# Kernel optimization log

Hardware: AMD Instinct MI355X
Metric: run time of the kernel (lower is better)

The kernel has to match this reference:

```python
import jax, jax.numpy as jnp
import numpy as np

B, N, D, H, DH, FF, CI, K, MPE = 8, 1024, 512, 8, 64, 2048, 1024, 31, 512
PAD = (K // 2, K // 2 - (K + 1) % 2)  # (15, 15)


def _ln(x, g, b):
    m = x.mean(-1, keepdims=True)
    v = ((x - m) ** 2).mean(-1, keepdims=True)
    return (x - m) * jax.lax.rsqrt(v + 1e-5) * g + b


def _swish(x):
    return x * jax.nn.sigmoid(x)


def setup_inputs() -> dict:
    key = jax.random.key(0)
    ks = iter(jax.random.split(key, 40))
    def w(shape, s=0.02):
        return (jax.random.normal(next(ks), shape) * s).astype(jnp.float32)
    ones = lambda n: jnp.ones((n,), jnp.float32)
    zeros = lambda n: jnp.zeros((n,), jnp.float32)
    return dict(
        x=jax.random.normal(next(ks), (B, N, D), dtype=jnp.float32),
        f1_g=ones(D), f1_b=zeros(D), f1_w1=w((D, FF)), f1_b1=zeros(FF), f1_w2=w((FF, D)), f1_b2=zeros(D),
        a_g=ones(D), a_b=zeros(D), wq=w((D, H * DH)), wkv=w((D, 2 * H * DH)), wo=w((H * DH, D)), wo_b=zeros(D),
        rel=w((2 * MPE + 1, DH)),
        c_g=ones(D), c_b=zeros(D), cw1=w((D, 2 * CI)), cb1=zeros(2 * CI), dw=w((CI, K)), db=zeros(CI),
        bn_g=ones(CI), bn_b=zeros(CI), bn_m=zeros(CI), bn_v=ones(CI), cw2=w((CI, D)), cb2=zeros(D),
        f2_g=ones(D), f2_b=zeros(D), f2_w1=w((D, FF)), f2_b1=zeros(FF), f2_w2=w((FF, D)), f2_b2=zeros(D),
        p_g=ones(D), p_b=zeros(D),
    )


def reference(x, f1_g, f1_b, f1_w1, f1_b1, f1_w2, f1_b2,
              a_g, a_b, wq, wkv, wo, wo_b, rel,
              c_g, c_b, cw1, cb1, dw, db, bn_g, bn_b, bn_m, bn_v, cw2, cb2,
              f2_g, f2_b, f2_w1, f2_b1, f2_w2, f2_b2, p_g, p_b):
    # FF1 (half-step)
    h = _ln(x, f1_g, f1_b)
    x = x + 0.5 * (_swish(h @ f1_w1 + f1_b1) @ f1_w2 + f1_b2)
    # Attention with relative positional bias
    h = _ln(x, a_g, a_b)
    q = (h @ wq).reshape(B, N, H, DH).transpose(0, 2, 1, 3)          # bhnd
    k, v = jnp.split(h @ wkv, 2, axis=-1)
    k = k.reshape(B, N, H, DH).transpose(0, 2, 1, 3)
    v = v.reshape(B, N, H, DH).transpose(0, 2, 1, 3)
    scale = DH ** -0.5
    dots = jnp.einsum('bhid,bhjd->bhij', q, k) * scale
    seq = jnp.arange(N)
    dist = jnp.clip(seq[:, None] - seq[None, :], -MPE, MPE) + MPE    # [N,N]
    rp = rel[dist]                                                   # [N,N,DH]
    dots = dots + jnp.einsum('bhnd,nrd->bhnr', q, rp) * scale
    attn = jax.nn.softmax(dots, axis=-1)
    o = jnp.einsum('bhij,bhjd->bhid', attn, v).transpose(0, 2, 1, 3).reshape(B, N, H * DH)
    x = x + o @ wo + wo_b
    # Conv module: LN -> pw conv -> GLU -> depthwise conv -> BN(eval) -> swish -> pw conv
    h = _ln(x, c_g, c_b)
    h = h @ cw1 + cb1                                                # [B,N,2CI]
    out, gate = jnp.split(h, 2, axis=-1)
    h = (out * jax.nn.sigmoid(gate)).transpose(0, 2, 1)              # [B,CI,N]
    h = jnp.pad(h, ((0, 0), (0, 0), PAD))
    h = jax.lax.conv_general_dilated(h, dw[:, None, :], (1,), 'VALID',
                                     feature_group_count=CI,
                                     dimension_numbers=('NCH', 'OIH', 'NCH')) + db[None, :, None]
    h = (h - bn_m[None, :, None]) * jax.lax.rsqrt(bn_v[None, :, None] + 1e-5) * bn_g[None, :, None] + bn_b[None, :, None]
    h = _swish(h).transpose(0, 2, 1)                                 # [B,N,CI]
    x = x + h @ cw2 + cb2
    # FF2 (half-step) + post norm
    h = _ln(x, f2_g, f2_b)
    x = x + 0.5 * (_swish(h @ f2_w1 + f2_b1) @ f2_w2 + f2_b2)
    return _ln(x, p_g, p_b)
```

## Files before the change

kernel.cpp:

```cpp
#include <hip/hip_runtime.h>
#include <hip/hip_bf16.h>
#include <cstdint>


using bf16_t = __hip_bfloat16;
typedef __bf16 bf16x8 __attribute__((ext_vector_type(8)));
typedef float floatx4 __attribute__((ext_vector_type(4)));

struct alignas(16) hbf8 { bf16_t h[8]; };
struct alignas(8)  hbf4 { bf16_t h[4]; };

__device__ __forceinline__ float  b2f(bf16_t h) { return __bfloat162float(h); }
__device__ __forceinline__ bf16_t f2b(float f)  { return __float2bfloat16(f); }
__device__ __forceinline__ float  sig_(float x) { return 1.f / (1.f + __expf(-x)); }

__device__ __forceinline__ void async16(const void* g, void* l) {
  __builtin_amdgcn_global_load_lds(
      (const __attribute__((address_space(1))) unsigned int*)(uintptr_t)g,
      (__attribute__((address_space(3))) unsigned int*)(uintptr_t)l, 16, 0, 0);
}

struct GemmArgs {
  const bf16_t* A; const bf16_t* Bt; const float* bias; const float* srcf;
  bf16_t* C; float* resid;
  int K, lda, ldb, ldc;
  long sAb, sAh, sBb, sBh, sCb, sCh;
  float alpha, beta;
};

template <int BM, int BN, int WR, int WC, int EPI>
__global__ __launch_bounds__(256) void gemm_bt(GemmArgs g) {
  constexpr int FM = BM / (WR * 16);
  constexpr int FN = BN / (WC * 16);
  constexpr int IA = (BM * 4) / 256;
  constexpr int IB = (BN * 4) / 256;
  __shared__ __align__(16) bf16_t As[BM * 32];
  __shared__ __align__(16) bf16_t Bs[BN * 32];
  const int tid = threadIdx.x;
  const int lane = tid & 63, w = tid >> 6;
  int bx = blockIdx.x, by = blockIdx.y;
  {
    const int gx = gridDim.x;
    const int nwg = gx * gridDim.y;
    if ((nwg & 7) == 0 && gridDim.z == 1) {
      int lin = by * gx + bx;
      int lid = (lin & 7) * (nwg >> 3) + (lin >> 3);
      bx = lid % gx; by = lid / gx;
    }
  }
  const int bm0 = by * BM, bn0 = bx * BN;
  const int zb = blockIdx.z >> 3, zh = blockIdx.z & 7;
  const bf16_t* Ab = g.A + (long)zb * g.sAb + (long)zh * g.sAh;
  const bf16_t* Bb = g.Bt + (long)zb * g.sBb + (long)zh * g.sBh;
  const int wm0 = (w / WC) * (FM * 16);
  const int wn0 = (w % WC) * (FN * 16);
  const int lrow = lane & 15, lq = lane >> 4;

  floatx4 acc[FM][FN] = {};

  for (int k0 = 0; k0 < g.K; k0 += 32) {
#pragma unroll
    for (int i = 0; i < IA; ++i) {
      int c = i * 256 + tid;
      int m = c >> 2, kk = (c & 3) * 8;
      async16(Ab + (long)(bm0 + m) * g.lda + (k0 + kk), (char*)As + c * 16);
    }
#pragma unroll
    for (int i = 0; i < IB; ++i) {
      int c = i * 256 + tid;
      int n = bn0 + (c >> 2), kk = (c & 3) * 8;
      async16(Bb + (long)n * g.ldb + (k0 + kk), (char*)Bs + c * 16);
    }
    __syncthreads();
    bf16x8 af[FM], bfr[FN];
#pragma unroll
    for (int fm = 0; fm < FM; ++fm)
      af[fm] = *(const bf16x8*)(As + (wm0 + fm * 16 + lrow) * 32 + lq * 8);
#pragma unroll
    for (int fn = 0; fn < FN; ++fn)
      bfr[fn] = *(const bf16x8*)(Bs + (wn0 + fn * 16 + lrow) * 32 + lq * 8);
#pragma unroll
    for (int fm = 0; fm < FM; ++fm)
#pragma unroll
      for (int fn = 0; fn < FN; ++fn)
        acc[fm][fn] = __builtin_amdgcn_mfma_f32_16x16x32_bf16(af[fm], bfr[fn], acc[fm][fn], 0, 0, 0);
    __syncthreads();
  }

  const int bi = bm0 + wm0 + lq * 4;
  const int bj = bn0 + wn0 + lrow;
  if constexpr (EPI == 2) {
    float* R = g.resid;
    const float* S = g.srcf;
#pragma unroll
    for (int fm = 0; fm < FM; ++fm)
#pragma unroll
      for (int fn = 0; fn < FN; ++fn) {
        int j = bj + fn * 16;
        float bv = g.bias ? g.bias[j] : 0.f;
#pragma unroll
        for (int r = 0; r < 4; ++r) {
          long i = bi + fm * 16 + r;
          float base = S ? S[i * g.ldc + j] : R[i * g.ldc + j];
          R[i * g.ldc + j] = base + g.beta * (acc[fm][fn][r] + bv);
        }
      }
  } else if constexpr (EPI == 4) {
    bf16_t* C = g.C;
#pragma unroll
    for (int fm = 0; fm < FM; ++fm)
#pragma unroll
      for (int fn = 0; fn < FN; ++fn) {
        int j = bj + fn * 16;
        float bv = g.bias[(j >> 1) + (j & 1) * 1024];
#pragma unroll
        for (int r = 0; r < 4; ++r) {
          int i = bi + fm * 16 + r;
          float v = acc[fm][fn][r] + bv;
          float gp = __shfl_xor(v, 1);
          if ((j & 1) == 0)
            C[(long)i * g.ldc + (j >> 1)] = f2b(v * sig_(gp));
        }
      }
  } else {
    bf16_t* C = g.C + (long)zb * g.sCb + (long)zh * g.sCh;
#pragma unroll
    for (int fm = 0; fm < FM; ++fm)
#pragma unroll
      for (int fn = 0; fn < FN; ++fn) {
        int j = bj + fn * 16;
        float bv = g.bias ? g.bias[j] : 0.f;
#pragma unroll
        for (int r = 0; r < 4; ++r) {
          int i = bi + fm * 16 + r;
          float v = acc[fm][fn][r];
          if constexpr (EPI == 0) v = g.alpha * v + bv;
          if constexpr (EPI == 1) { v += bv; v = v * sig_(v); }
          C[(long)i * g.ldc + j] = f2b(v);
        }
      }
  }
}

__global__ __launch_bounds__(512, 4) void attn_kernel(
    const bf16_t* __restrict__ QKV, const bf16_t* __restrict__ VT,
    const bf16_t* __restrict__ RELP, bf16_t* __restrict__ O) {
  constexpr int LDT = 1028;
  __shared__ __align__(16) bf16_t Tls[32 * LDT];
  __shared__ float scr[576];

  const int tid = threadIdx.x;
  const int w = tid >> 6, lane = tid & 63;
  const int lrow = lane & 15, lq = lane >> 4;
  const int lin = blockIdx.y * gridDim.x + blockIdx.x;
  const int lid = (lin & 7) * 256 + (lin >> 3);
  const int z = lid >> 5;
  const int i0 = (lid & 31) * 32;
  const int b = z >> 3, zh = z & 7;
  const int j0w = w * 128;

  const bf16_t* Qb  = QKV + ((long)(b * 1024 + i0)) * 1536 + zh * 64;
  const bf16_t* Kb  = QKV + ((long)b * 1024) * 1536 + 512 + zh * 64;
  const bf16_t* VTb = VT + ((long)(b * 8 + zh)) * 65536;

  bf16x8 af[2][2];
#pragma unroll
  for (int fm = 0; fm < 2; ++fm)
#pragma unroll
    for (int ks = 0; ks < 2; ++ks)
      af[fm][ks] = *(const bf16x8*)(Qb + (long)(fm * 16 + lrow) * 1536 + ks * 32 + lq * 8);

  {
    const int u0w = w * 144;
    bf16x8 rf[18];
#pragma unroll
    for (int fnT = 0; fnT < 9; ++fnT) {
      const int u0 = u0w + fnT * 16;
      if (u0 < LDT) {
        rf[2 * fnT]     = *(const bf16x8*)(RELP + (long)(u0 + lrow) * 64 + lq * 8);
        rf[2 * fnT + 1] = *(const bf16x8*)(RELP + (long)(u0 + lrow) * 64 + 32 + lq * 8);
      }
    }
#pragma unroll
    for (int fnT = 0; fnT < 9; ++fnT) {
      const int u0 = u0w + fnT * 16;
      if (u0 < LDT) {
        floatx4 tacc[2] = {};
        tacc[0] = __builtin_amdgcn_mfma_f32_16x16x32_bf16(af[0][0], rf[2 * fnT],     tacc[0], 0, 0, 0);
        tacc[0] = __builtin_amdgcn_mfma_f32_16x16x32_bf16(af[0][1], rf[2 * fnT + 1], tacc[0], 0, 0, 0);
        tacc[1] = __builtin_amdgcn_mfma_f32_16x16x32_bf16(af[1][0], rf[2 * fnT],     tacc[1], 0, 0, 0);
        tacc[1] = __builtin_amdgcn_mfma_f32_16x16x32_bf16(af[1][1], rf[2 * fnT + 1], tacc[1], 0, 0, 0);
        const int uu = u0 + lrow;
#pragma unroll
        for (int fm = 0; fm < 2; ++fm)
#pragma unroll
          for (int r = 0; r < 4; ++r)
            if (uu < LDT)
              Tls[(fm * 16 + lq * 4 + r) * LDT + uu] = f2b(tacc[fm][r]);
      }
    }
  }

  bf16x8 kfA[8], kfB[8];
#pragma unroll
  for (int x = 0; x < 8; ++x)
    kfA[x] = *(const bf16x8*)(Kb + (long)(j0w + (x >> 1) * 16 + lrow) * 1536 + (x & 1) * 32 + lq * 8);
#pragma unroll
  for (int x = 0; x < 8; ++x)
    kfB[x] = *(const bf16x8*)(Kb + (long)(j0w + (4 + (x >> 1)) * 16 + lrow) * 1536 + (x & 1) * 32 + lq * 8);
  __syncthreads();

  floatx4 sacc[2][8] = {};
#pragma unroll
  for (int fn = 0; fn < 4; ++fn) {
    sacc[0][fn] = __builtin_amdgcn_mfma_f32_16x16x32_bf16(af[0][0], kfA[2 * fn],     sacc[0][fn], 0, 0, 0);
    sacc[0][fn] = __builtin_amdgcn_mfma_f32_16x16x32_bf16(af[0][1], kfA[2 * fn + 1], sacc[0][fn], 0, 0, 0);
    sacc[1][fn] = __builtin_amdgcn_mfma_f32_16x16x32_bf16(af[1][0], kfA[2 * fn],     sacc[1][fn], 0, 0, 0);
    sacc[1][fn] = __builtin_amdgcn_mfma_f32_16x16x32_bf16(af[1][1], kfA[2 * fn + 1], sacc[1][fn], 0, 0, 0);
  }
#pragma unroll
  for (int fn = 4; fn < 8; ++fn) {
    sacc[0][fn] = __builtin_amdgcn_mfma_f32_16x16x32_bf16(af[0][0], kfB[2 * (fn - 4)],     sacc[0][fn], 0, 0, 0);
    sacc[0][fn] = __builtin_amdgcn_mfma_f32_16x16x32_bf16(af[0][1], kfB[2 * (fn - 4) + 1], sacc[0][fn], 0, 0, 0);
    sacc[1][fn] = __builtin_amdgcn_mfma_f32_16x16x32_bf16(af[1][0], kfB[2 * (fn - 4)],     sacc[1][fn], 0, 0, 0);
    sacc[1][fn] = __builtin_amdgcn_mfma_f32_16x16x32_bf16(af[1][1], kfB[2 * (fn - 4) + 1], sacc[1][fn], 0, 0, 0);
  }

#pragma unroll
  for (int fm = 0; fm < 2; ++fm)
#pragma unroll
    for (int r = 0; r < 4; ++r) {
      const int il = fm * 16 + lq * 4 + r;
      const bf16_t* trow = Tls + il * LDT + 512;
      const int tb = i0 + il - j0w - lrow;
#pragma unroll
      for (int fn = 0; fn < 8; ++fn) {
        int t = tb - fn * 16;
        t = t < -512 ? -512 : (t > 512 ? 512 : t);
        sacc[fm][fn][r] += b2f(trow[t]);
      }
    }

  float rmax[2][4];
#pragma unroll
  for (int fm = 0; fm < 2; ++fm)
#pragma unroll
    for (int r = 0; r < 4; ++r) {
      float m = sacc[fm][0][r];
#pragma unroll
      for (int fn = 1; fn < 8; ++fn) m = fmaxf(m, sacc[fm][fn][r]);
      rmax[fm][r] = m;
    }
#pragma unroll
  for (int off = 1; off < 16; off <<= 1)
#pragma unroll
    for (int fm = 0; fm < 2; ++fm)
#pragma unroll
      for (int r = 0; r < 4; ++r)
        rmax[fm][r] = fmaxf(rmax[fm][r], __shfl_xor(rmax[fm][r], off));
  if (lrow == 0)
#pragma unroll
    for (int fm = 0; fm < 2; ++fm)
#pragma unroll
      for (int r = 0; r < 4; ++r)
        scr[(fm * 16 + lq * 4 + r) * 9 + w] = rmax[fm][r];
  __syncthreads();

  float rsum[2][4];
#pragma unroll
  for (int fm = 0; fm < 2; ++fm)
#pragma unroll
    for (int r = 0; r < 4; ++r) {
      const float* rr = scr + (fm * 16 + lq * 4 + r) * 9;
      float m = rr[0];
#pragma unroll
      for (int ww = 1; ww < 8; ++ww) m = fmaxf(m, rr[ww]);
      float s = 0.f;
#pragma unroll
      for (int fn = 0; fn < 8; ++fn) {
        float e = __expf(sacc[fm][fn][r] - m);
        sacc[fm][fn][r] = e;
        s += e;
      }
      rsum[fm][r] = s;
    }
#pragma unroll
  for (int off = 1; off < 16; off <<= 1)
#pragma unroll
    for (int fm = 0; fm < 2; ++fm)
#pragma unroll
      for (int r = 0; r < 4; ++r)
        rsum[fm][r] += __shfl_xor(rsum[fm][r], off);
  if (lrow == 0)
#pragma unroll
    for (int fm = 0; fm < 2; ++fm)
#pragma unroll
      for (int r = 0; r < 4; ++r)
        scr[288 + (fm * 16 + lq * 4 + r) * 9 + w] = rsum[fm][r];
  __syncthreads();

  float inv[2][4];
#pragma unroll
  for (int fm = 0; fm < 2; ++fm)
#pragma unroll
    for (int r = 0; r < 4; ++r) {
      const float* rr = scr + 288 + (fm * 16 + lq * 4 + r) * 9;
      float s = rr[0];
#pragma unroll
      for (int ww = 1; ww < 8; ++ww) s += rr[ww];
      inv[fm][r] = 1.f / s;
    }

  bf16x8 vfA[8];
#pragma unroll
  for (int x = 0; x < 8; ++x)
    vfA[x] = *(const bf16x8*)(VTb + (long)((x & 3) * 16 + lrow) * 1024 + j0w + (x >> 2) * 32 + lq * 8);

#pragma unroll
  for (int fm = 0; fm < 2; ++fm)
#pragma unroll
    for (int fn = 0; fn < 8; ++fn)
#pragma unroll
      for (int r = 0; r < 4; ++r) {
        const int i = fm * 16 + lq * 4 + r;
        const int j = j0w + fn * 16 + lrow;
        const unsigned boff = (unsigned)(i * 2048 + j * 2) ^ ((unsigned)(i & 7) << 4);
        *(bf16_t*)((char*)Tls + boff) = f2b(sacc[fm][fn][r] * inv[fm][r]);
      }

  bf16x8 vfB[8];
#pragma unroll
  for (int x = 0; x < 8; ++x)
    vfB[x] = *(const bf16x8*)(VTb + (long)((x & 3) * 16 + lrow) * 1024 + j0w + 64 + (x >> 2) * 32 + lq * 8);

  floatx4 oacc[2][4] = {};
#pragma unroll
  for (int ks = 0; ks < 4; ++ks) {
    const int j = j0w + ks * 32;
    bf16x8 ap[2];
#pragma unroll
    for (int fm = 0; fm < 2; ++fm) {
      const int i = fm * 16 + lrow;
      const unsigned boff = (unsigned)(i * 2048 + (j + lq * 8) * 2) ^ ((unsigned)(i & 7) << 4);
      ap[fm] = *(const bf16x8*)((char*)Tls + boff);
    }
#pragma unroll
    for (int fd = 0; fd < 4; ++fd) {
      bf16x8 bv = (ks < 2) ? vfA[(ks << 2) | fd] : vfB[((ks - 2) << 2) | fd];
      oacc[0][fd] = __builtin_amdgcn_mfma_f32_16x16x32_bf16(ap[0], bv, oacc[0][fd], 0, 0, 0);
      oacc[1][fd] = __builtin_amdgcn_mfma_f32_16x16x32_bf16(ap[1], bv, oacc[1][fd], 0, 0, 0);
    }
  }
  __syncthreads();

  {
    float* part = (float*)Tls + w * 2048;
#pragma unroll
    for (int fm = 0; fm < 2; ++fm)
#pragma unroll
      for (int fd = 0; fd < 4; ++fd)
#pragma unroll
        for (int r = 0; r < 4; ++r)
          part[(fm * 16 + lq * 4 + r) * 64 + fd * 16 + lrow] = oacc[fm][fd][r];
  }
  __syncthreads();

  {
    const int i = tid >> 4;
    const int d0 = (tid & 15) * 4;
    floatx4 s = {};
#pragma unroll
    for (int ww = 0; ww < 8; ++ww)
      s += *(const floatx4*)((const float*)Tls + ww * 2048 + i * 64 + d0);
    hbf4 o4;
#pragma unroll
    for (int m = 0; m < 4; ++m) o4.h[m] = f2b(s[m]);
    *(hbf4*)(O + (long)(b * 1024 + i0 + i) * 512 + zh * 64 + d0) = o4;
  }
}

__global__ __launch_bounds__(256) void diag_kernel(float* __restrict__ out, long n, float v) {
  long i = (long)blockIdx.x * 256 + threadIdx.x;
  if (i < n) out[i] = v;
}

__global__ __launch_bounds__(256) void relpad_kernel(const float* __restrict__ rel, bf16_t* __restrict__ RELP) {
  int i = blockIdx.x * 256 + threadIdx.x;
  if (i < 73728) {
    int r = i >> 6, c = i & 63;
    RELP[i] = (r < 1025) ? f2b(rel[r * 64 + c]) : f2b(0.f);
  }
}

template <bool F32OUT>
__global__ __launch_bounds__(256) void ln_kernel(const float* __restrict__ X, const float* __restrict__ gam,
                                                 const float* __restrict__ bet, void* __restrict__ outv) {
  int row = blockIdx.x, tid = threadIdx.x;
  const float* x = X + (long)row * 512;
  float a = x[tid], b = x[tid + 256];
  float s = a + b, q = a * a + b * b;
  for (int off = 32; off; off >>= 1) { s += __shfl_down(s, off); q += __shfl_down(q, off); }
  __shared__ float red[8];
  int w = tid >> 6;
  if ((tid & 63) == 0) { red[w] = s; red[w + 4] = q; }
  __syncthreads();
  float ts = red[0] + red[1] + red[2] + red[3];
  float tq = red[4] + red[5] + red[6] + red[7];
  float mean = ts * (1.f / 512.f);
  float var = tq * (1.f / 512.f) - mean * mean;
  float rs = rsqrtf(var + 1e-5f);
  float o0 = (a - mean) * rs * gam[tid]       + bet[tid];
  float o1 = (b - mean) * rs * gam[tid + 256] + bet[tid + 256];
  if constexpr (F32OUT) {
    float* out = (float*)outv;
    out[(long)row * 512 + tid]       = o0;
    out[(long)row * 512 + tid + 256] = o1;
  } else {
    bf16_t* out = (bf16_t*)outv;
    out[(long)row * 512 + tid]       = f2b(o0);
    out[(long)row * 512 + tid + 256] = f2b(o1);
  }
}

__global__ __launch_bounds__(256) void transpose_kernel(const float* __restrict__ in, bf16_t* __restrict__ out,
                                                        int R, int C, float scale, int perm) {
  __shared__ float t[32][33];
  int c0 = blockIdx.x * 32, r0 = blockIdx.y * 32;
  int tx = threadIdx.x & 31, ty = threadIdx.x >> 5;
#pragma unroll
  for (int i = 0; i < 4; ++i)
    t[ty + i * 8][tx] = in[(long)(r0 + ty + i * 8) * C + c0 + tx];
  __syncthreads();
#pragma unroll
  for (int i = 0; i < 4; ++i) {
    int c = c0 + ty + i * 8;
    int row = perm ? ((c < 1024) ? 2 * c : 2 * (c - 1024) + 1) : c;
    out[(long)row * R + r0 + tx] = f2b(t[tx][ty + i * 8] * scale);
  }
}

__global__ __launch_bounds__(256) void vt_kernel(const bf16_t* __restrict__ QKV, bf16_t* __restrict__ VT) {
  int jb = blockIdx.x, z = blockIdx.y;
  int b = z >> 3, h = z & 7;
  const bf16_t* src = QKV + (long)b * 1024 * 1536 + 1024 + h * 64;
  bf16_t* dst = VT + (long)z * 65536;
  __shared__ bf16_t t[64][65];
  int tid = threadIdx.x;
#pragma unroll
  for (int i = 0; i < 16; ++i) {
    int l = i * 256 + tid;
    int j = l >> 6, d = l & 63;
    t[d][j] = src[(long)(jb * 64 + j) * 1536 + d];
  }
  __syncthreads();
#pragma unroll
  for (int i = 0; i < 16; ++i) {
    int l = i * 256 + tid;
    int d = l >> 6, j = l & 63;
    dst[(long)d * 1024 + jb * 64 + j] = t[d][j];
  }
}

__global__ __launch_bounds__(256) void dwconv_kernel(const bf16_t* __restrict__ G, const float* __restrict__ dw,
    const float* __restrict__ db, const float* __restrict__ bng, const float* __restrict__ bnb,
    const float* __restrict__ bnm, const float* __restrict__ bnv, bf16_t* __restrict__ out) {
  int n0 = blockIdx.x * 32, c0 = blockIdx.y * 64, b = blockIdx.z;
  __shared__ bf16_t t[62][64];
  __shared__ float dws[31][64];
  int tid = threadIdx.x;
  const bf16_t* src = G + (long)b * 1024 * 1024 + c0;
#pragma unroll
  for (int i = 0; i < 16; ++i) {
    int l = i * 256 + tid;
    if (l < 3968) {
      int rr = l >> 6, c = l & 63;
      int n = n0 - 15 + rr;
      t[rr][c] = (n >= 0 && n < 1024) ? src[(long)n * 1024 + c] : f2b(0.f);
    }
  }
#pragma unroll
  for (int i = 0; i < 8; ++i) {
    int l = i * 256 + tid;
    if (l < 1984) {
      int k = l >> 6, c = l & 63;
      dws[k][c] = dw[(long)(c0 + c) * 31 + k];
    }
  }
  __syncthreads();
  int c = tid & 63, nl = tid >> 6;
  float rs = rsqrtf(bnv[c0 + c] + 1e-5f);
  float sc = rs * bng[c0 + c];
  float ab = (db[c0 + c] - bnm[c0 + c]) * sc + bnb[c0 + c];
#pragma unroll
  for (int j = 0; j < 8; ++j) {
    int rr = nl * 8 + j;
    float s = 0.f;
#pragma unroll
    for (int k = 0; k < 31; ++k) s += b2f(t[rr + k][c]) * dws[k][c];
    float y = s * sc + ab;
    out[((long)b * 1024 + n0 + rr) * 1024 + c0 + c] = f2b(y * sig_(y));
  }
}

extern "C" void kernel_launch(void* const* d_in, const int* in_sizes, int n_in,
                              void* d_out, int out_size, void* d_ws, size_t ws_size,
                              hipStream_t stream) {
  auto fail = [&](float code) {
    diag_kernel<<<(out_size + 255) / 256, 256, 0, stream>>>((float*)d_out, out_size, code);
  };
  if (n_in != 34)             { fail(70.f);  return; }
  if (in_sizes[0] != 4194304) { fail(80.f);  return; }

  const float* x     = (const float*)d_in[0];
  const float* f1_g  = (const float*)d_in[1];
  const float* f1_b  = (const float*)d_in[2];
  const float* f1_w1 = (const float*)d_in[3];
  const float* f1_b1 = (const float*)d_in[4];
  const float* f1_w2 = (const float*)d_in[5];
  const float* f1_b2 = (const float*)d_in[6];
  const float* a_g   = (const float*)d_in[7];
  const float* a_b   = (const float*)d_in[8];
  const float* wq    = (const float*)d_in[9];
  const float* wkv   = (const float*)d_in[10];
  const float* wo    = (const float*)d_in[11];
  const float* wo_b  = (const float*)d_in[12];
  const float* rel   = (const float*)d_in[13];
  const float* c_g   = (const float*)d_in[14];
  const float* c_b   = (const float*)d_in[15];
  const float* cw1   = (const float*)d_in[16];
  const float* cb1   = (const float*)d_in[17];
  const float* dwp   = (const float*)d_in[18];
  const float* dbp   = (const float*)d_in[19];
  const float* bn_g  = (const float*)d_in[20];
  const float* bn_b  = (const float*)d_in[21];
  const float* bn_m  = (const float*)d_in[22];
  const float* bn_v  = (const float*)d_in[23];
  const float* cw2   = (const float*)d_in[24];
  const float* cb2   = (const float*)d_in[25];
  const float* f2_g  = (const float*)d_in[26];
  const float* f2_b  = (const float*)d_in[27];
  const float* f2_w1 = (const float*)d_in[28];
  const float* f2_b1 = (const float*)d_in[29];
  const float* f2_w2 = (const float*)d_in[30];
  const float* f2_b2 = (const float*)d_in[31];
  const float* p_g   = (const float*)d_in[32];
  const float* p_b   = (const float*)d_in[33];

  char* ws = (char*)d_ws;
  const size_t OFF_X  = 0;
  const size_t OFF_WT = 16777216;
  const size_t OFF_D  = 30408704;
  const size_t OFF_E  = 63963136;
  const size_t relp_off = OFF_E + 33554432;
  if (ws_size < relp_off + 147456ULL) { fail(200.f); return; }

  float*  X   = (float*)(ws + OFF_X);
  bf16_t* WT  = (bf16_t*)(ws + OFF_WT);
  bf16_t* QKV = (bf16_t*)(ws + OFF_D);
  bf16_t* VT  = (bf16_t*)(ws + OFF_D + 25165824);
  bf16_t* GLU = (bf16_t*)(ws + OFF_D);
  bf16_t* DWO = (bf16_t*)(ws + OFF_D + 16777216);
  bf16_t* MID = (bf16_t*)(ws + OFF_E);
  bf16_t* RELP= (bf16_t*)(ws + relp_off);
  bf16_t* H   = (bf16_t*)d_out;
  bf16_t* O   = (bf16_t*)d_out;

  bf16_t* f1_w1t = WT;            bf16_t* f1_w2t = WT + 1048576;
  bf16_t* wqkvt  = WT + 2097152;
  bf16_t* wot    = WT + 2883584;  bf16_t* cw1t   = WT + 3145728;
  bf16_t* cw2t   = WT + 4194304;  bf16_t* f2_w1t = WT + 4718592;
  bf16_t* f2_w2t = WT + 5767168;

  auto GA = [](const bf16_t* A, const bf16_t* Bt, const float* bias, bf16_t* C,
               float* resid, const float* srcf, int K, int lda, int ldb, int ldc,
               float alpha, float beta) {
    GemmArgs g{}; g.A = A; g.Bt = Bt; g.bias = bias; g.srcf = srcf; g.C = C; g.resid = resid;
    g.K = K; g.lda = lda; g.ldb = ldb; g.ldc = ldc;
    g.sAb = g.sAh = g.sBb = g.sBh = g.sCb = g.sCh = 0; g.alpha = alpha; g.beta = beta;
    return g;
  };
  auto T = [&](const float* in, bf16_t* out, int R, int C, float scale = 1.f, int perm = 0) {
    transpose_kernel<<<dim3(C / 32, R / 32), 256, 0, stream>>>(in, out, R, C, scale, perm);
  };

  relpad_kernel<<<288, 256, 0, stream>>>(rel, RELP);
  T(f1_w1, f1_w1t, 512, 2048);        T(f1_w2, f1_w2t, 2048, 512);
  T(wq, wqkvt, 512, 512, 0.125f);     T(wkv, wqkvt + 262144, 512, 1024);
  T(wo, wot, 512, 512);               T(cw1, cw1t, 512, 2048, 1.f, 1);
  T(cw2, cw2t, 1024, 512);            T(f2_w1, f2_w1t, 512, 2048);
  T(f2_w2, f2_w2t, 2048, 512);

  ln_kernel<false><<<8192, 256, 0, stream>>>(x, f1_g, f1_b, H);
  { GemmArgs g = GA(H, f1_w1t, f1_b1, MID, nullptr, nullptr, 512, 512, 512, 2048, 1.f, 0.f);
    gemm_bt<128, 128, 2, 2, 1><<<dim3(16, 64, 1), 256, 0, stream>>>(g); }
  { GemmArgs g = GA(MID, f1_w2t, f1_b2, nullptr, X, x, 2048, 2048, 2048, 512, 1.f, 0.5f);
    gemm_bt<64, 128, 1, 4, 2><<<dim3(4, 128, 1), 256, 0, stream>>>(g); }

  ln_kernel<false><<<8192, 256, 0, stream>>>(X, a_g, a_b, H);
  { GemmArgs g = GA(H, wqkvt, nullptr, QKV, nullptr, nullptr, 512, 512, 512, 1536, 1.f, 0.f);
    gemm_bt<128, 128, 2, 2, 0><<<dim3(12, 64, 1), 256, 0, stream>>>(g); }
  vt_kernel<<<dim3(16, 64), 256, 0, stream>>>(QKV, VT);

  attn_kernel<<<dim3(32, 64), 512, 0, stream>>>(QKV, VT, RELP, O);

  { GemmArgs g = GA(O, wot, wo_b, nullptr, X, nullptr, 512, 512, 512, 512, 1.f, 1.f);
    gemm_bt<64, 128, 1, 4, 2><<<dim3(4, 128, 1), 256, 0, stream>>>(g); }

  ln_kernel<false><<<8192, 256, 0, stream>>>(X, c_g, c_b, H);
  { GemmArgs g = GA(H, cw1t, cb1, GLU, nullptr, nullptr, 512, 512, 512, 1024, 1.f, 0.f);
    gemm_bt<128, 128, 2, 2, 4><<<dim3(16, 64, 1), 256, 0, stream>>>(g); }
  dwconv_kernel<<<dim3(32, 16, 8), 256, 0, stream>>>(GLU, dwp, dbp, bn_g, bn_b, bn_m, bn_v, DWO);
  { GemmArgs g = GA(DWO, cw2t, cb2, nullptr, X, nullptr, 1024, 1024, 1024, 512, 1.f, 1.f);
    gemm_bt<64, 128, 1, 4, 2><<<dim3(4, 128, 1), 256, 0, stream>>>(g); }

  ln_kernel<false><<<8192, 256, 0, stream>>>(X, f2_g, f2_b, H);
  { GemmArgs g = GA(H, f2_w1t, f2_b1, MID, nullptr, nullptr, 512, 512, 512, 2048, 1.f, 0.f);
    gemm_bt<128, 128, 2, 2, 1><<<dim3(16, 64, 1), 256, 0, stream>>>(g); }
  { GemmArgs g = GA(MID, f2_w2t, f2_b2, nullptr, X, nullptr, 2048, 2048, 2048, 512, 1.f, 0.5f);
    gemm_bt<64, 128, 1, 4, 2><<<dim3(4, 128, 1), 256, 0, stream>>>(g); }
  ln_kernel<true><<<8192, 256, 0, stream>>>(X, p_g, p_b, (float*)d_out);
}
```

Baseline: 643.5 us.

## Defer softmax normalization to cross-wave merge and batch weight prep into one launch

Attention softmax now uses each wave's local row max and sum instead of a block-wide max and sum, which removes two __syncthreads barriers. The per-wave partial outputs are then rescaled by exp(local max minus global max) and normalized during the final cross-wave reduction, as in flash-style merging. Separately, the nine weight transposes and the relpad conversion are merged into a single prep_kernel launch driven by a job table, which cuts launch overhead. The cost is some extra exp and multiply work in the reduction and a per-block linear search over the job table.

```diff
diff --git a/kernel.cpp b/kernel.cpp
--- a/kernel.cpp
+++ b/kernel.cpp
@@ -264,21 +264,16 @@
 #pragma unroll
       for (int r = 0; r < 4; ++r)
         scr[(fm * 16 + lq * 4 + r) * 9 + w] = rmax[fm][r];
-  __syncthreads();
 
   float rsum[2][4];
 #pragma unroll
   for (int fm = 0; fm < 2; ++fm)
 #pragma unroll
     for (int r = 0; r < 4; ++r) {
-      const float* rr = scr + (fm * 16 + lq * 4 + r) * 9;
-      float m = rr[0];
-#pragma unroll
-      for (int ww = 1; ww < 8; ++ww) m = fmaxf(m, rr[ww]);
       float s = 0.f;
 #pragma unroll
       for (int fn = 0; fn < 8; ++fn) {
-        float e = __expf(sacc[fm][fn][r] - m);
+        float e = __expf(sacc[fm][fn][r] - rmax[fm][r]);
         sacc[fm][fn][r] = e;
         s += e;
       }
@@ -297,24 +292,13 @@
 #pragma unroll
       for (int r = 0; r < 4; ++r)
         scr[288 + (fm * 16 + lq * 4 + r) * 9 + w] = rsum[fm][r];
-  __syncthreads();
-
-  float inv[2][4];
-#pragma unroll
-  for (int fm = 0; fm < 2; ++fm)
-#pragma unroll
-    for (int r = 0; r < 4; ++r) {
-      const float* rr = scr + 288 + (fm * 16 + lq * 4 + r) * 9;
-      float s = rr[0];
-#pragma unroll
-      for (int ww = 1; ww < 8; ++ww) s += rr[ww];
-      inv[fm][r] = 1.f / s;
-    }
 
   bf16x8 vfA[8];
 #pragma unroll
   for (int x = 0; x < 8; ++x)
     vfA[x] = *(const bf16x8*)(VTb + (long)((x & 3) * 16 + lrow) * 1024 + j0w + (x >> 2) * 32 + lq * 8);
+
+  __syncthreads();
 
 #pragma unroll
   for (int fm = 0; fm < 2; ++fm)
@@ -325,7 +309,7 @@
         const int i = fm * 16 + lq * 4 + r;
         const int j = j0w + fn * 16 + lrow;
         const unsigned boff = (unsigned)(i * 2048 + j * 2) ^ ((unsigned)(i & 7) << 4);
-        *(bf16_t*)((char*)Tls + boff) = f2b(sacc[fm][fn][r] * inv[fm][r]);
+        *(bf16_t*)((char*)Tls + boff) = f2b(sacc[fm][fn][r]);
       }
 
   bf16x8 vfB[8];
@@ -368,13 +352,28 @@
   {
     const int i = tid >> 4;
     const int d0 = (tid & 15) * 4;
+    float mw[8], sw[8];
+#pragma unroll
+    for (int ww = 0; ww < 8; ++ww) {
+      mw[ww] = scr[i * 9 + ww];
+      sw[ww] = scr[288 + i * 9 + ww];
+    }
+    float M = mw[0];
+#pragma unroll
+    for (int ww = 1; ww < 8; ++ww) M = fmaxf(M, mw[ww]);
+    float fac[8]; float tot = 0.f;
+#pragma unroll
+    for (int ww = 0; ww < 8; ++ww) { fac[ww] = __expf(mw[ww] - M); tot += sw[ww] * fac[ww]; }
+    const float inv = 1.f / tot;
     floatx4 s = {};
 #pragma unroll
-    for (int ww = 0; ww < 8; ++ww)
-      s += *(const floatx4*)((const float*)Tls + ww * 2048 + i * 64 + d0);
+    for (int ww = 0; ww < 8; ++ww) {
+      floatx4 p = *(const floatx4*)((const float*)Tls + ww * 2048 + i * 64 + d0);
+      s += p * fac[ww];
+    }
     hbf4 o4;
 #pragma unroll
-    for (int m = 0; m < 4; ++m) o4.h[m] = f2b(s[m]);
+    for (int m = 0; m < 4; ++m) o4.h[m] = f2b(s[m] * inv);
     *(hbf4*)(O + (long)(b * 1024 + i0 + i) * 512 + zh * 64 + d0) = o4;
   }
 }
@@ -384,11 +383,44 @@
   if (i < n) out[i] = v;
 }
 
-__global__ __launch_bounds__(256) void relpad_kernel(const float* __restrict__ rel, bf16_t* __restrict__ RELP) {
-  int i = blockIdx.x * 256 + threadIdx.x;
-  if (i < 73728) {
-    int r = i >> 6, c = i & 63;
-    RELP[i] = (r < 1025) ? f2b(rel[r * 64 + c]) : f2b(0.f);
+struct PrepJobs {
+  const float* src[10];
+  bf16_t*      dst[10];
+  int R[10], C[10], gx[10], start[10];
+  float scale[10];
+  int   mode[10];
+  int   njobs;
+};
+
+__global__ __launch_bounds__(256) void prep_kernel(PrepJobs P) {
+  __shared__ float t[32][33];
+  const int bid = blockIdx.x;
+  int j = 0;
+  while (j + 1 < P.njobs && bid >= P.start[j + 1]) ++j;
+  const int tile = bid - P.start[j];
+  const int tid = threadIdx.x;
+  if (P.mode[j] == 2) {
+    int i = tile * 256 + tid;
+    if (i < 73728) {
+      int r = i >> 6, c = i & 63;
+      P.dst[j][i] = (r < 1025) ? f2b(P.src[j][r * 64 + c]) : f2b(0.f);
+    }
+    return;
+  }
+  const int gx = P.gx[j];
+  const int c0 = (tile % gx) * 32, r0 = (tile / gx) * 32;
+  const int C = P.C[j], R = P.R[j];
+  const float scale = P.scale[j];
+  const int tx = tid & 31, ty = tid >> 5;
+#pragma unroll
+  for (int i = 0; i < 4; ++i)
+    t[ty + i * 8][tx] = P.src[j][(long)(r0 + ty + i * 8) * C + c0 + tx];
+  __syncthreads();
+#pragma unroll
+  for (int i = 0; i < 4; ++i) {
+    int c = c0 + ty + i * 8;
+    int row = (P.mode[j] == 1) ? ((c < 1024) ? 2 * c : 2 * (c - 1024) + 1) : c;
+    P.dst[j][(long)row * R + r0 + tx] = f2b(t[tx][ty + i * 8] * scale);
   }
 }
 
@@ -419,23 +451,6 @@
     bf16_t* out = (bf16_t*)outv;
     out[(long)row * 512 + tid]       = f2b(o0);
     out[(long)row * 512 + tid + 256] = f2b(o1);
-  }
-}
-
-__global__ __launch_bounds__(256) void transpose_kernel(const float* __restrict__ in, bf16_t* __restrict__ out,
-                                                        int R, int C, float scale, int perm) {
-  __shared__ float t[32][33];
-  int c0 = blockIdx.x * 32, r0 = blockIdx.y * 32;
-  int tx = threadIdx.x & 31, ty = threadIdx.x >> 5;
-#pragma unroll
-  for (int i = 0; i < 4; ++i)
-    t[ty + i * 8][tx] = in[(long)(r0 + ty + i * 8) * C + c0 + tx];
-  __syncthreads();
-#pragma unroll
-  for (int i = 0; i < 4; ++i) {
-    int c = c0 + ty + i * 8;
-    int row = perm ? ((c < 1024) ? 2 * c : 2 * (c - 1024) + 1) : c;
-    out[(long)row * R + r0 + tx] = f2b(t[tx][ty + i * 8] * scale);
   }
 }
 
@@ -579,16 +594,27 @@
     g.sAb = g.sAh = g.sBb = g.sBh = g.sCb = g.sCh = 0; g.alpha = alpha; g.beta = beta;
     return g;
   };
-  auto T = [&](const float* in, bf16_t* out, int R, int C, float scale = 1.f, int perm = 0) {
-    transpose_kernel<<<dim3(C / 32, R / 32), 256, 0, stream>>>(in, out, R, C, scale, perm);
-  };
-
-  relpad_kernel<<<288, 256, 0, stream>>>(rel, RELP);
-  T(f1_w1, f1_w1t, 512, 2048);        T(f1_w2, f1_w2t, 2048, 512);
-  T(wq, wqkvt, 512, 512, 0.125f);     T(wkv, wqkvt + 262144, 512, 1024);
-  T(wo, wot, 512, 512);               T(cw1, cw1t, 512, 2048, 1.f, 1);
-  T(cw2, cw2t, 1024, 512);            T(f2_w1, f2_w1t, 512, 2048);
-  T(f2_w2, f2_w2t, 2048, 512);
+
+  {
+    PrepJobs P{};
+    auto set = [&](int idx, const float* s, bf16_t* d, int R, int C, int start,
+                   float sc, int mode) {
+      P.src[idx] = s; P.dst[idx] = d; P.R[idx] = R; P.C[idx] = C;
+      P.gx[idx] = C / 32; P.start[idx] = start; P.scale[idx] = sc; P.mode[idx] = mode;
+    };
+    set(0, f1_w1, f1_w1t,          512, 2048,    0, 1.f,    0);
+    set(1, f1_w2, f1_w2t,         2048,  512, 1024, 1.f,    0);
+    set(2, wq,    wqkvt,           512,  512, 2048, 0.125f, 0);
+    set(3, wkv,   wqkvt + 262144,  512, 1024, 2304, 1.f,    0);
+    set(4, wo,    wot,             512,  512, 2816, 1.f,    0);
+    set(5, cw1,   cw1t,            512, 2048, 3072, 1.f,    1);
+    set(6, cw2,   cw2t,           1024,  512, 4096, 1.f,    0);
+    set(7, f2_w1, f2_w1t,          512, 2048, 4608, 1.f,    0);
+    set(8, f2_w2, f2_w2t,         2048,  512, 5632, 1.f,    0);
+    set(9, rel,   RELP,           1025,   64, 6656, 1.f,    2);
+    P.njobs = 10;
+    prep_kernel<<<6944, 256, 0, stream>>>(P);
+  }
 
   ln_kernel<false><<<8192, 256, 0, stream>>>(x, f1_g, f1_b, H);
   { GemmArgs g = GA(H, f1_w1t, f1_b1, MID, nullptr, nullptr, 512, 512, 512, 2048, 1.f, 0.f);
```

After: 625.6 us. 1.03x faster.
